# Optimization experiments

Hardware: AMD Instinct MI355X
Metric: run time of the kernel (lower is better)

The kernel has to match this reference:

```python
import jax, jax.numpy as jnp
import numpy as np

B, IN_CAPS, IN_DIM = 256, 1152, 8
OUT_CAPS, OUT_DIM = 10, 16
NUM_ROUTING = 3


def setup_inputs() -> dict:
    key = jax.random.key(0)
    k_u, k_w = jax.random.split(key)
    u = jax.random.normal(k_u, (B, IN_CAPS, IN_DIM), dtype=jnp.float32)
    # nn.init.normal_(W, mean=0.0, std=0.01); torch shape [1, in, out, out_dim, in_dim]
    W = 0.01 * jax.random.normal(k_w, (IN_CAPS, OUT_CAPS, OUT_DIM, IN_DIM), dtype=jnp.float32)
    return {"u": u, "W": W}


def _squash(s, eps=1e-8):
    # v = (||s||^2 / (1 + ||s||^2)) * s / ||s||, along last dim
    sq = jnp.sum(s * s, axis=-1, keepdims=True)
    return (sq / (1.0 + sq)) * s / jnp.sqrt(sq + eps)


def reference(u, W):
    # u: [b, i, d_in]; W: [i, o, d_out, d_in] -> u_hat: [b, i, o, d_out]
    u_hat = jnp.einsum("iodk,bik->biod", W, u)
    b = jnp.zeros((u.shape[0], IN_CAPS, OUT_CAPS), dtype=u.dtype)
    v = None
    for it in range(NUM_ROUTING):
        c = jax.nn.softmax(b, axis=2)                       # [b, i, o]
        s = jnp.einsum("bio,biod->bod", c, u_hat)           # weighted sum over input caps
        v = _squash(s)                                      # [b, o, d_out]
        if it < NUM_ROUTING - 1:
            b = b + jnp.einsum("biod,bod->bio", u_hat, v)   # agreement
    return v
```

## Files before the change

### kernel.cpp

```cpp
#include <hip/hip_runtime.h>
#include <hip/hip_fp16.h>

#define B_SZ  256
#define IC    1152
#define ID    8
#define OC    10
#define ODIM  16
#define OD160 160
#define CH    20

__global__ __launch_bounds__(256) void uhat_kernel(
    const float* __restrict__ u, const float* __restrict__ W,
    uint4* __restrict__ uhat)
{
    const int i = blockIdx.x;
    const int t = threadIdx.x;
    const int h = t >> 5;
    const int c = t & 31;
    const bool act = (c < CH);
    const int cc = act ? c : (CH - 1);

    __shared__ float4 ulds[B_SZ * 2];

    {
        const float4* ub = (const float4*)(u + ((size_t)t * IC + i) * ID);
        ulds[t * 2]     = ub[0];
        ulds[t * 2 + 1] = ub[1];
    }

    float4 Wr[16];
    {
        const float4* wsrc = (const float4*)(W + (size_t)i * OD160 * ID) + cc * 16;
        #pragma unroll
        for (int m = 0; m < 16; ++m) Wr[m] = wsrc[m];
    }
    __syncthreads();

    #pragma unroll 2
    for (int iter = 0; iter < 32; ++iter) {
        const int b = iter * 8 + h;
        float4 u0 = ulds[b * 2], u1 = ulds[b * 2 + 1];
        float o[8];
        #pragma unroll
        for (int j = 0; j < 8; ++j) {
            const float4 wa = Wr[j * 2], wb = Wr[j * 2 + 1];
            o[j] = wa.x * u0.x + wa.y * u0.y + wa.z * u0.z + wa.w * u0.w
                 + wb.x * u1.x + wb.y * u1.y + wb.z * u1.z + wb.w * u1.w;
        }
        if (act) {
            union { __half2 h2[4]; uint4 q; } pk;
            pk.h2[0] = __floats2half2_rn(o[0], o[1]);
            pk.h2[1] = __floats2half2_rn(o[2], o[3]);
            pk.h2[2] = __floats2half2_rn(o[4], o[5]);
            pk.h2[3] = __floats2half2_rn(o[6], o[7]);
            uhat[((size_t)b * IC + i) * CH + c] = pk.q;
        }
    }
}

__global__ __launch_bounds__(1024) void routing_kernel(
    const uint4* __restrict__ uhat, float4* __restrict__ out)
{
    const int b  = blockIdx.x;
    const int t  = threadIdx.x;
    const int wv = t >> 6;
    const int ln = t & 63;
    const int h  = ln >> 5;
    const int c  = ln & 31;
    const bool act = (c < CH);
    const int cc = act ? c : (CH - 1);

    __shared__ float4 sred[16][2 * CH];
    __shared__ float4 vlds[2 * CH];

    const int NI = IC / 16;
    const int i0 = wv * NI;

    const uint4* base = uhat + (size_t)b * IC * CH + cc;

    float vs[8];
    float4 vout = make_float4(0.f, 0.f, 0.f, 0.f);

    for (int p = 0; p < 3; ++p) {
        float s[8] = {0.f, 0.f, 0.f, 0.f, 0.f, 0.f, 0.f, 0.f};

        uint4 c0 = base[(size_t)(i0 + h) * CH];
        uint4 c1 = base[(size_t)(i0 + 2 + h) * CH];

        for (int it = 0; it < NI / 2; ++it) {
            uint4 nxt = c1;
            if (it + 2 < NI / 2) nxt = base[(size_t)(i0 + 2 * (it + 2) + h) * CH];

            const __half2* hp = (const __half2*)&c0;
            float2 f0 = __half22float2(hp[0]);
            float2 f1 = __half22float2(hp[1]);
            float2 f2 = __half22float2(hp[2]);
            float2 f3 = __half22float2(hp[3]);

            if (p == 0) {
                s[0] += f0.x; s[1] += f0.y; s[2] += f1.x; s[3] += f1.y;
                s[4] += f2.x; s[5] += f2.y; s[6] += f3.x; s[7] += f3.y;
            } else {
                float a = f0.x * vs[0] + f0.y * vs[1] + f1.x * vs[2] + f1.y * vs[3]
                        + f2.x * vs[4] + f2.y * vs[5] + f3.x * vs[6] + f3.y * vs[7];
                a += __shfl_xor(a, 1);
                float e = act ? __expf(a) : 0.0f;
                float Z = e;
                Z += __shfl_xor(Z, 2);
                Z += __shfl_xor(Z, 4);
                Z += __shfl_xor(Z, 8);
                Z += __shfl_xor(Z, 16);
                float cf = __fdividef(e, Z);
                s[0] += cf * f0.x; s[1] += cf * f0.y; s[2] += cf * f1.x; s[3] += cf * f1.y;
                s[4] += cf * f2.x; s[5] += cf * f2.y; s[6] += cf * f3.x; s[7] += cf * f3.y;
            }
            c0 = c1; c1 = nxt;
        }

        #pragma unroll
        for (int j = 0; j < 8; ++j) s[j] += __shfl_xor(s[j], 32);

        if (h == 0 && act) {
            sred[wv][2 * c]     = make_float4(s[0], s[1], s[2], s[3]);
            sred[wv][2 * c + 1] = make_float4(s[4], s[5], s[6], s[7]);
        }
        __syncthreads();

        if (wv == 0 && ln < 2 * CH) {
            float4 S = sred[0][ln];
            #pragma unroll
            for (int w2 = 1; w2 < 16; ++w2) {
                float4 q = sred[w2][ln];
                S.x += q.x; S.y += q.y; S.z += q.z; S.w += q.w;
            }
            if (p == 0) { S.x *= 0.1f; S.y *= 0.1f; S.z *= 0.1f; S.w *= 0.1f; }
            float n2 = S.x * S.x + S.y * S.y + S.z * S.z + S.w * S.w;
            n2 += __shfl_xor(n2, 1);
            n2 += __shfl_xor(n2, 2);
            float sc = (n2 / (1.0f + n2)) * rsqrtf(n2 + 1e-8f);
            float4 V = make_float4(S.x * sc, S.y * sc, S.z * sc, S.w * sc);
            vlds[ln] = V;
            vout = V;
        }
        __syncthreads();

        if (p < 2) {
            float4 q0 = vlds[2 * cc], q1 = vlds[2 * cc + 1];
            if (p == 0) {
                vs[0] = q0.x; vs[1] = q0.y; vs[2] = q0.z; vs[3] = q0.w;
                vs[4] = q1.x; vs[5] = q1.y; vs[6] = q1.z; vs[7] = q1.w;
            } else {
                vs[0] += q0.x; vs[1] += q0.y; vs[2] += q0.z; vs[3] += q0.w;
                vs[4] += q1.x; vs[5] += q1.y; vs[6] += q1.z; vs[7] += q1.w;
            }
        }
        __syncthreads();
    }

    if (wv == 0 && ln < 2 * CH) {
        out[(size_t)b * 2 * CH + ln] = vout;
    }
}

extern "C" void kernel_launch(void* const* d_in, const int* in_sizes, int n_in,
                              void* d_out, int out_size, void* d_ws, size_t ws_size,
                              hipStream_t stream)
{
    const float* u = (const float*)d_in[0];
    const float* W = (const float*)d_in[1];

    uint4* uhat = (uint4*)d_ws;

    uhat_kernel<<<IC, 256, 0, stream>>>(u, W, uhat);
    routing_kernel<<<B_SZ, 1024, 0, stream>>>(uhat, (float4*)d_out);
}
```

Before: 134.3 us.

## Fuse first routing pass into uhat kernel and remap routing lanes per output capsule

The u_hat kernel now tiles over (input-capsule chunk, batch chunk) and accumulates the uniform-coupling first-pass sum s0 into shared memory with atomics, then into a global buffer. A small squash kernel produces v0, and the routing kernel runs only the two remaining passes. Each lane now handles a full 16-dim output capsule, so the agreement dot product needs no cross-lane shuffle. This removes one full re-read of u_hat in exchange for many shared-memory float atomics, global atomics, an extra memset and an extra kernel launch.

```diff
diff --git a/kernel.cpp b/kernel.cpp
--- a/kernel.cpp
+++ b/kernel.cpp
@@ -6,159 +6,223 @@
 #define ID    8
 #define OC    10
 #define ODIM  16
-#define OD160 160
+#define ROWH  160
 #define CH    20
-
-__global__ __launch_bounds__(256) void uhat_kernel(
+#define BC    16
+#define ICH   32
+
+__global__ __launch_bounds__(256) void uhat_s0_kernel(
     const float* __restrict__ u, const float* __restrict__ W,
-    uint4* __restrict__ uhat)
-{
-    const int i = blockIdx.x;
+    uint4* __restrict__ uhat, float* __restrict__ s0g)
+{
+    const int bx     = blockIdx.x;
+    const int ic_blk = bx >> 4;
+    const int bc_blk = bx & 15;
+    const int i0 = ic_blk * ICH;
+    const int b0 = bc_blk * BC;
+
     const int t = threadIdx.x;
     const int h = t >> 5;
     const int c = t & 31;
     const bool act = (c < CH);
     const int cc = act ? c : (CH - 1);
-
-    __shared__ float4 ulds[B_SZ * 2];
-
-    {
-        const float4* ub = (const float4*)(u + ((size_t)t * IC + i) * ID);
-        ulds[t * 2]     = ub[0];
-        ulds[t * 2 + 1] = ub[1];
-    }
-
-    float4 Wr[16];
-    {
-        const float4* wsrc = (const float4*)(W + (size_t)i * OD160 * ID) + cc * 16;
-        #pragma unroll
-        for (int m = 0; m < 16; ++m) Wr[m] = wsrc[m];
+    const int par = h & 1;
+
+    __shared__ float4 ul[BC * ICH * 2];
+    __shared__ float  s0l[2][BC][ROWH];
+
+    for (int idx = t; idx < 2 * BC * ROWH; idx += 256) ((float*)s0l)[idx] = 0.f;
+
+    const float4* uf4 = (const float4*)u;
+    #pragma unroll
+    for (int r = 0; r < 4; ++r) {
+        int idx = t + 256 * r;
+        int bb = idx >> 6, rem = idx & 63, ii = rem >> 1, part = rem & 1;
+        ul[idx] = uf4[((size_t)(b0 + bb) * IC + (i0 + ii)) * 2 + part];
     }
     __syncthreads();
 
-    #pragma unroll 2
-    for (int iter = 0; iter < 32; ++iter) {
-        const int b = iter * 8 + h;
-        float4 u0 = ulds[b * 2], u1 = ulds[b * 2 + 1];
-        float o[8];
-        #pragma unroll
-        for (int j = 0; j < 8; ++j) {
-            const float4 wa = Wr[j * 2], wb = Wr[j * 2 + 1];
-            o[j] = wa.x * u0.x + wa.y * u0.y + wa.z * u0.z + wa.w * u0.w
-                 + wb.x * u1.x + wb.y * u1.y + wb.z * u1.z + wb.w * u1.w;
-        }
-        if (act) {
-            union { __half2 h2[4]; uint4 q; } pk;
-            pk.h2[0] = __floats2half2_rn(o[0], o[1]);
-            pk.h2[1] = __floats2half2_rn(o[2], o[3]);
-            pk.h2[2] = __floats2half2_rn(o[4], o[5]);
-            pk.h2[3] = __floats2half2_rn(o[6], o[7]);
-            uhat[((size_t)b * IC + i) * CH + c] = pk.q;
-        }
-    }
-}
-
-__global__ __launch_bounds__(1024) void routing_kernel(
-    const uint4* __restrict__ uhat, float4* __restrict__ out)
+    const float4* wf4 = (const float4*)W;
+
+    for (int t4 = 0; t4 < 4; ++t4) {
+        const int ii = h + 8 * t4;
+        const int i  = i0 + ii;
+
+        float4 Wr[16];
+        {
+            const float4* wsrc = wf4 + (size_t)i * 320 + cc * 16;
+            #pragma unroll
+            for (int m = 0; m < 16; ++m) Wr[m] = wsrc[m];
+        }
+
+        #pragma unroll 2
+        for (int bb = 0; bb < BC; ++bb) {
+            float4 u0 = ul[(bb * ICH + ii) * 2];
+            float4 u1 = ul[(bb * ICH + ii) * 2 + 1];
+            float o[8];
+            #pragma unroll
+            for (int j = 0; j < 8; ++j) {
+                float4 wa = Wr[2 * j], wb = Wr[2 * j + 1];
+                o[j] = wa.x * u0.x + wa.y * u0.y + wa.z * u0.z + wa.w * u0.w
+                     + wb.x * u1.x + wb.y * u1.y + wb.z * u1.z + wb.w * u1.w;
+            }
+            if (act) {
+                union { __half2 h2[4]; uint4 q; } pk;
+                pk.h2[0] = __floats2half2_rn(o[0], o[1]);
+                pk.h2[1] = __floats2half2_rn(o[2], o[3]);
+                pk.h2[2] = __floats2half2_rn(o[4], o[5]);
+                pk.h2[3] = __floats2half2_rn(o[6], o[7]);
+                uhat[((size_t)(b0 + bb) * IC + i) * CH + c] = pk.q;
+                #pragma unroll
+                for (int j = 0; j < 8; ++j)
+                    atomicAdd(&s0l[par][bb][8 * c + j], o[j]);
+            }
+        }
+    }
+    __syncthreads();
+
+    if (t < ROWH) {
+        for (int bb = 0; bb < BC; ++bb)
+            atomicAdd(&s0g[(size_t)(b0 + bb) * ROWH + t],
+                      s0l[0][bb][t] + s0l[1][bb][t]);
+    }
+}
+
+__global__ __launch_bounds__(192) void squash0_kernel(
+    const float* __restrict__ s0g, float* __restrict__ v0g)
+{
+    const int b = blockIdx.x, t = threadIdx.x;
+    if (t < ROWH) {
+        float S = 0.1f * s0g[(size_t)b * ROWH + t];
+        float n2 = S * S;
+        n2 += __shfl_xor(n2, 1);
+        n2 += __shfl_xor(n2, 2);
+        n2 += __shfl_xor(n2, 4);
+        n2 += __shfl_xor(n2, 8);
+        float sc = (n2 / (1.0f + n2)) * rsqrtf(n2 + 1e-8f);
+        v0g[(size_t)b * ROWH + t] = S * sc;
+    }
+}
+
+__global__ __launch_bounds__(1024) void routing2_kernel(
+    const uint4* __restrict__ uhat, const float* __restrict__ v0g,
+    float* __restrict__ out)
 {
     const int b  = blockIdx.x;
     const int t  = threadIdx.x;
     const int wv = t >> 6;
     const int ln = t & 63;
-    const int h  = ln >> 5;
-    const int c  = ln & 31;
-    const bool act = (c < CH);
-    const int cc = act ? c : (CH - 1);
-
-    __shared__ float4 sred[16][2 * CH];
-    __shared__ float4 vlds[2 * CH];
-
-    const int NI = IC / 16;
-    const int i0 = wv * NI;
-
-    const uint4* base = uhat + (size_t)b * IC * CH + cc;
-
-    float vs[8];
-    float4 vout = make_float4(0.f, 0.f, 0.f, 0.f);
-
-    for (int p = 0; p < 3; ++p) {
-        float s[8] = {0.f, 0.f, 0.f, 0.f, 0.f, 0.f, 0.f, 0.f};
-
-        uint4 c0 = base[(size_t)(i0 + h) * CH];
-        uint4 c1 = base[(size_t)(i0 + 2 + h) * CH];
-
-        for (int it = 0; it < NI / 2; ++it) {
-            uint4 nxt = c1;
-            if (it + 2 < NI / 2) nxt = base[(size_t)(i0 + 2 * (it + 2) + h) * CH];
-
-            const __half2* hp = (const __half2*)&c0;
-            float2 f0 = __half22float2(hp[0]);
-            float2 f1 = __half22float2(hp[1]);
-            float2 f2 = __half22float2(hp[2]);
-            float2 f3 = __half22float2(hp[3]);
-
-            if (p == 0) {
-                s[0] += f0.x; s[1] += f0.y; s[2] += f1.x; s[3] += f1.y;
-                s[4] += f2.x; s[5] += f2.y; s[6] += f3.x; s[7] += f3.y;
-            } else {
-                float a = f0.x * vs[0] + f0.y * vs[1] + f1.x * vs[2] + f1.y * vs[3]
-                        + f2.x * vs[4] + f2.y * vs[5] + f3.x * vs[6] + f3.y * vs[7];
-                a += __shfl_xor(a, 1);
-                float e = act ? __expf(a) : 0.0f;
-                float Z = e;
-                Z += __shfl_xor(Z, 2);
-                Z += __shfl_xor(Z, 4);
-                Z += __shfl_xor(Z, 8);
-                Z += __shfl_xor(Z, 16);
-                float cf = __fdividef(e, Z);
-                s[0] += cf * f0.x; s[1] += cf * f0.y; s[2] += cf * f1.x; s[3] += cf * f1.y;
-                s[4] += cf * f2.x; s[5] += cf * f2.y; s[6] += cf * f3.x; s[7] += cf * f3.y;
-            }
-            c0 = c1; c1 = nxt;
-        }
-
+    const int ii = ln >> 4;
+    const int os = ln & 15;
+    const bool act = (os < OC);
+    const int o  = act ? os : (OC - 1);
+
+    __shared__ float sred[16][164];
+    __shared__ float vl[ROWH];
+
+    const char* base = (const char*)uhat + (size_t)b * IC * 320 + o * 32;
+
+    float v[16];
+    {
+        const float4* vp = (const float4*)(v0g + (size_t)b * ROWH + o * 16);
+        float4 q0 = vp[0], q1 = vp[1], q2 = vp[2], q3 = vp[3];
+        v[0]=q0.x; v[1]=q0.y; v[2]=q0.z; v[3]=q0.w;
+        v[4]=q1.x; v[5]=q1.y; v[6]=q1.z; v[7]=q1.w;
+        v[8]=q2.x; v[9]=q2.y; v[10]=q2.z; v[11]=q2.w;
+        v[12]=q3.x; v[13]=q3.y; v[14]=q3.z; v[15]=q3.w;
+    }
+
+    const int ibase = wv * 72 + ii;
+
+    for (int p = 1; p <= 2; ++p) {
+        float s[16];
         #pragma unroll
-        for (int j = 0; j < 8; ++j) s[j] += __shfl_xor(s[j], 32);
-
-        if (h == 0 && act) {
-            sred[wv][2 * c]     = make_float4(s[0], s[1], s[2], s[3]);
-            sred[wv][2 * c + 1] = make_float4(s[4], s[5], s[6], s[7]);
+        for (int j = 0; j < 16; ++j) s[j] = 0.f;
+
+        uint4 A0 = *(const uint4*)(base + (size_t)ibase * 320);
+        uint4 A1 = *(const uint4*)(base + (size_t)ibase * 320 + 16);
+        uint4 B0 = *(const uint4*)(base + (size_t)(ibase + 4) * 320);
+        uint4 B1 = *(const uint4*)(base + (size_t)(ibase + 4) * 320 + 16);
+
+        #pragma unroll 2
+        for (int it = 0; it < 18; ++it) {
+            uint4 N0 = B0, N1 = B1;
+            if (it + 2 < 18) {
+                const char* np = base + (size_t)(ibase + (it + 2) * 4) * 320;
+                N0 = *(const uint4*)np;
+                N1 = *(const uint4*)(np + 16);
+            }
+
+            float r[16];
+            const __half2* hp0 = (const __half2*)&A0;
+            const __half2* hp1 = (const __half2*)&A1;
+            #pragma unroll
+            for (int q = 0; q < 4; ++q) {
+                float2 f = __half22float2(hp0[q]);
+                float2 g = __half22float2(hp1[q]);
+                r[2 * q]     = f.x; r[2 * q + 1] = f.y;
+                r[8 + 2 * q] = g.x; r[9 + 2 * q] = g.y;
+            }
+
+            float a = 0.f;
+            #pragma unroll
+            for (int j = 0; j < 16; ++j) a += r[j] * v[j];
+
+            float e = act ? __expf(a) : 0.f;
+            float Z = e;
+            Z += __shfl_xor(Z, 1);
+            Z += __shfl_xor(Z, 2);
+            Z += __shfl_xor(Z, 4);
+            Z += __shfl_xor(Z, 8);
+            float cf = __fdividef(e, Z);
+
+            #pragma unroll
+            for (int j = 0; j < 16; ++j) s[j] += cf * r[j];
+
+            A0 = B0; A1 = B1; B0 = N0; B1 = N1;
+        }
+
+        #pragma unroll
+        for (int j = 0; j < 16; ++j) {
+            s[j] += __shfl_xor(s[j], 16);
+            s[j] += __shfl_xor(s[j], 32);
+        }
+        if (ln < 16 && act) {
+            float4* dst = (float4*)&sred[wv][os * 16];
+            dst[0] = make_float4(s[0],  s[1],  s[2],  s[3]);
+            dst[1] = make_float4(s[4],  s[5],  s[6],  s[7]);
+            dst[2] = make_float4(s[8],  s[9],  s[10], s[11]);
+            dst[3] = make_float4(s[12], s[13], s[14], s[15]);
         }
         __syncthreads();
 
-        if (wv == 0 && ln < 2 * CH) {
-            float4 S = sred[0][ln];
-            #pragma unroll
-            for (int w2 = 1; w2 < 16; ++w2) {
-                float4 q = sred[w2][ln];
-                S.x += q.x; S.y += q.y; S.z += q.z; S.w += q.w;
-            }
-            if (p == 0) { S.x *= 0.1f; S.y *= 0.1f; S.z *= 0.1f; S.w *= 0.1f; }
-            float n2 = S.x * S.x + S.y * S.y + S.z * S.z + S.w * S.w;
+        if (t < ROWH) {
+            float S = 0.f;
+            #pragma unroll
+            for (int w2 = 0; w2 < 16; ++w2) S += sred[w2][t];
+            float n2 = S * S;
             n2 += __shfl_xor(n2, 1);
             n2 += __shfl_xor(n2, 2);
+            n2 += __shfl_xor(n2, 4);
+            n2 += __shfl_xor(n2, 8);
             float sc = (n2 / (1.0f + n2)) * rsqrtf(n2 + 1e-8f);
-            float4 V = make_float4(S.x * sc, S.y * sc, S.z * sc, S.w * sc);
-            vlds[ln] = V;
-            vout = V;
+            vl[t] = S * sc;
         }
         __syncthreads();
 
-        if (p < 2) {
-            float4 q0 = vlds[2 * cc], q1 = vlds[2 * cc + 1];
-            if (p == 0) {
-                vs[0] = q0.x; vs[1] = q0.y; vs[2] = q0.z; vs[3] = q0.w;
-                vs[4] = q1.x; vs[5] = q1.y; vs[6] = q1.z; vs[7] = q1.w;
-            } else {
-                vs[0] += q0.x; vs[1] += q0.y; vs[2] += q0.z; vs[3] += q0.w;
-                vs[4] += q1.x; vs[5] += q1.y; vs[6] += q1.z; vs[7] += q1.w;
-            }
-        }
-        __syncthreads();
-    }
-
-    if (wv == 0 && ln < 2 * CH) {
-        out[(size_t)b * 2 * CH + ln] = vout;
+        if (p == 1) {
+            const float4* vp = (const float4*)&vl[o * 16];
+            float4 q0 = vp[0], q1 = vp[1], q2 = vp[2], q3 = vp[3];
+            v[0]+=q0.x; v[1]+=q0.y; v[2]+=q0.z; v[3]+=q0.w;
+            v[4]+=q1.x; v[5]+=q1.y; v[6]+=q1.z; v[7]+=q1.w;
+            v[8]+=q2.x; v[9]+=q2.y; v[10]+=q2.z; v[11]+=q2.w;
+            v[12]+=q3.x; v[13]+=q3.y; v[14]+=q3.z; v[15]+=q3.w;
+            __syncthreads();
+        }
+    }
+
+    if (t < 2 * CH) {
+        ((float4*)out)[(size_t)b * 2 * CH + t] = ((const float4*)vl)[t];
     }
 }
 
@@ -169,8 +233,14 @@
     const float* u = (const float*)d_in[0];
     const float* W = (const float*)d_in[1];
 
-    uint4* uhat = (uint4*)d_ws;
-
-    uhat_kernel<<<IC, 256, 0, stream>>>(u, W, uhat);
-    routing_kernel<<<B_SZ, 1024, 0, stream>>>(uhat, (float4*)d_out);
-}
+    const size_t UHAT_BYTES = (size_t)B_SZ * IC * CH * 16;
+    char* ws = (char*)d_ws;
+    uint4* uhat = (uint4*)ws;
+    float* s0g  = (float*)(ws + UHAT_BYTES);
+    float* v0g  = (float*)(ws + UHAT_BYTES + (size_t)B_SZ * ROWH * 4);
+
+    hipMemsetAsync(s0g, 0, (size_t)B_SZ * ROWH * 4, stream);
+    uhat_s0_kernel<<<(IC / ICH) * (B_SZ / BC), 256, 0, stream>>>(u, W, uhat, s0g);
+    squash0_kernel<<<B_SZ, 192, 0, stream>>>(s0g, v0g);
+    routing2_kernel<<<B_SZ, 1024, 0, stream>>>(uhat, v0g, (float*)d_out);
+}
```

New measurement: 410.3 us. 3.06x slower.
